# Kernel optimization log

Hardware: AMD Instinct MI355X
Metric: run time of the kernel (lower is better)

## Reference

```python
import jax, jax.numpy as jnp
import numpy as np

N_NODES = 100000
N_EDGES = 1600000
IN_F = 128
OUT_F = 64


def setup_inputs() -> dict:
    key = jax.random.key(0)
    k1, k2, k3, k4, k5, k6 = jax.random.split(key, 6)
    stdv = 1.0 / np.sqrt(OUT_F)
    return {
        "input": jax.random.normal(k1, (N_NODES, IN_F), dtype=jnp.float32),
        "weights": jax.random.uniform(k2, (IN_F, OUT_F), minval=-stdv, maxval=stdv, dtype=jnp.float32),
        "bias": jax.random.uniform(k3, (OUT_F,), minval=-stdv, maxval=stdv, dtype=jnp.float32),
        "adj_vals": jax.random.uniform(k4, (N_EDGES,), dtype=jnp.float32),
        "adj_rows": jax.random.randint(k5, (N_EDGES,), 0, N_NODES, dtype=jnp.int32),
        "adj_cols": jax.random.randint(k6, (N_EDGES,), 0, N_NODES, dtype=jnp.int32),
    }


def reference(input, weights, bias, adj_vals, adj_rows, adj_cols):
    # Dense transform: support = input @ W   -> [N, out_features]
    support = jnp.matmul(input, weights)
    # Sparse adjacency matmul (COO SpMM): out[r] += v * support[c]
    msgs = adj_vals[:, None] * support[adj_cols]          # [E, out_features]
    output = jax.ops.segment_sum(msgs, adj_rows, num_segments=N_NODES)
    # Fused bias epilogue
    return output + bias
```

## Files before the change

kernel.cpp:

```cpp
#include <hip/hip_runtime.h>
#include <hip/hip_bf16.h>

#define N_NODES 100000
#define IN_F 128
#define OUT_F 64
#define BROWS 64
#define NB 1563
#define BIN_TILE 4096
#define CSB_CAP 2048

__device__ __forceinline__ unsigned short f2bf(float x) {
    unsigned u = __float_as_uint(x);
    u += 0x7FFFu + ((u >> 16) & 1u);
    return (unsigned short)(u >> 16);
}
__device__ __forceinline__ float bf2f(unsigned short s) {
    return __uint_as_float(((unsigned)s) << 16);
}

__global__ __launch_bounds__(256) void gemm_count_kernel(
    const float* __restrict__ in, const float* __restrict__ W,
    unsigned short* __restrict__ support,
    const int* __restrict__ rows, int* __restrict__ cnt,
    int nE, int gemmBlocks)
{
    __shared__ float Alds[64 * 129];
    __shared__ int histL[NB];
    const int t = threadIdx.x;

    if ((int)blockIdx.x >= gemmBlocks) {
        for (int i = t; i < NB; i += 256) histL[i] = 0;
        __syncthreads();
        const int cb = blockIdx.x - gemmBlocks;
        for (int e = cb * 256 + t; e < nE; e += 256 * 256)
            atomicAdd(&histL[rows[e] >> 6], 1);
        __syncthreads();
        for (int i = t; i < NB; i += 256) {
            int h = histL[i];
            if (h) atomicAdd(&cnt[i], h);
        }
        return;
    }

    const long row0 = (long)blockIdx.x * 64;

    #pragma unroll
    for (int i = 0; i < 8; ++i) {
        int fi = t + i * 256;
        int r  = fi >> 5;
        int k4 = (fi & 31) << 2;
        float4 v = make_float4(0.f, 0.f, 0.f, 0.f);
        if (row0 + r < N_NODES)
            v = *(const float4*)(in + (row0 + r) * IN_F + k4);
        Alds[r * 129 + k4 + 0] = v.x;
        Alds[r * 129 + k4 + 1] = v.y;
        Alds[r * 129 + k4 + 2] = v.z;
        Alds[r * 129 + k4 + 3] = v.w;
    }
    __syncthreads();

    const int lane = t & 63;
    const int c0   = __builtin_amdgcn_readfirstlane((t >> 6) << 4);
    const float* __restrict__ Wp = W + c0;

    float acc[16];
    #pragma unroll
    for (int i = 0; i < 16; ++i) acc[i] = 0.f;

    const float* Ar = Alds + lane * 129;
    for (int k = 0; k < IN_F; ++k) {
        const float a = Ar[k];
        const float4 w0 = *(const float4*)(Wp + k * OUT_F + 0);
        const float4 w1 = *(const float4*)(Wp + k * OUT_F + 4);
        const float4 w2 = *(const float4*)(Wp + k * OUT_F + 8);
        const float4 w3 = *(const float4*)(Wp + k * OUT_F + 12);
        acc[0]  = fmaf(a, w0.x, acc[0]);  acc[1]  = fmaf(a, w0.y, acc[1]);
        acc[2]  = fmaf(a, w0.z, acc[2]);  acc[3]  = fmaf(a, w0.w, acc[3]);
        acc[4]  = fmaf(a, w1.x, acc[4]);  acc[5]  = fmaf(a, w1.y, acc[5]);
        acc[6]  = fmaf(a, w1.z, acc[6]);  acc[7]  = fmaf(a, w1.w, acc[7]);
        acc[8]  = fmaf(a, w2.x, acc[8]);  acc[9]  = fmaf(a, w2.y, acc[9]);
        acc[10] = fmaf(a, w2.z, acc[10]); acc[11] = fmaf(a, w2.w, acc[11]);
        acc[12] = fmaf(a, w3.x, acc[12]); acc[13] = fmaf(a, w3.y, acc[13]);
        acc[14] = fmaf(a, w3.z, acc[14]); acc[15] = fmaf(a, w3.w, acc[15]);
    }

    const long orow = row0 + lane;
    if (orow < N_NODES) {
        unsigned up[8];
        #pragma unroll
        for (int i = 0; i < 8; ++i)
            up[i] = (unsigned)f2bf(acc[2 * i]) |
                    ((unsigned)f2bf(acc[2 * i + 1]) << 16);
        unsigned short* o = support + orow * OUT_F + c0;
        *(uint4*)(o + 0) = make_uint4(up[0], up[1], up[2], up[3]);
        *(uint4*)(o + 8) = make_uint4(up[4], up[5], up[6], up[7]);
    }
}

__global__ __launch_bounds__(256) void zero_kernel(int* __restrict__ p, int n)
{
    int i = blockIdx.x * 256 + threadIdx.x;
    if (i < n) p[i] = 0;
}

__global__ __launch_bounds__(256) void scan_kernel(
    const int* __restrict__ cnt, int* __restrict__ base,
    int* __restrict__ cursor, int nE)
{
    __shared__ int lds[256];
    const int t = threadIdx.x;
    const int i0 = t * 8;
    int c[8];
    int tot = 0;
    #pragma unroll
    for (int k = 0; k < 8; ++k) {
        c[k] = (i0 + k < NB) ? cnt[i0 + k] : 0;
        tot += c[k];
    }

    lds[t] = tot;
    __syncthreads();
    int sum = tot;
    #pragma unroll
    for (int off = 1; off < 256; off <<= 1) {
        int y = (t >= off) ? lds[t - off] : 0;
        __syncthreads();
        sum += y;
        lds[t] = sum;
        __syncthreads();
    }
    int run = sum - tot;

    #pragma unroll
    for (int k = 0; k < 8; ++k) {
        if (i0 + k < NB) { base[i0 + k] = run; cursor[i0 + k] = run; }
        run += c[k];
    }
    if (t == 0) base[NB] = nE;
}

__global__ __launch_bounds__(256) void bin_kernel(
    const int* __restrict__ rows, const int* __restrict__ cols,
    const float* __restrict__ vals, int* __restrict__ cursor,
    uint2* __restrict__ binned, int nE)
{
    __shared__ int hist[NB];
    __shared__ int lbase[NB];
    const int t  = threadIdx.x;
    const int tb = blockIdx.x * BIN_TILE;

    for (int i = t; i < NB; i += 256) hist[i] = 0;
    __syncthreads();

    int myr[16], myrank[16];
    #pragma unroll
    for (int i = 0; i < 16; ++i) {
        int e = tb + i * 256 + t;
        if (e < nE) {
            int r = rows[e];
            myr[i] = r;
            myrank[i] = atomicAdd(&hist[r >> 6], 1);
        } else myr[i] = -1;
    }
    __syncthreads();

    for (int i = t; i < NB; i += 256) {
        int h = hist[i];
        lbase[i] = h ? atomicAdd(&cursor[i], h) : 0;
    }
    __syncthreads();

    #pragma unroll
    for (int i = 0; i < 16; ++i) {
        int e = tb + i * 256 + t;
        if (e < nE) {
            int r = myr[i];
            unsigned pack = ((unsigned)(r & (BROWS - 1)) << 17) | (unsigned)cols[e];
            binned[lbase[r >> 6] + myrank[i]] =
                make_uint2(pack, __float_as_uint(vals[e]));
        }
    }
}

__global__ __launch_bounds__(1024, 2) void csr_spmm(
    const int* __restrict__ base, const uint2* __restrict__ binned,
    const unsigned short* __restrict__ support, const float* __restrict__ bias,
    float* __restrict__ out)
{
    __shared__ uint2 stage[CSB_CAP];
    __shared__ uint2 sorted[CSB_CAP];
    __shared__ int rh[BROWS], rs[BROWS + 1], rc[BROWS];
    const int t = threadIdx.x;
    const int b = blockIdx.x;
    const int s = base[b], e = base[b + 1];
    const int n = e - s;
    const int wid  = t >> 6;
    const int lane = t & 63;
    const int row0 = b * BROWS;

    if (t < BROWS) rh[t] = 0;
    __syncthreads();

    if (n <= CSB_CAP) {
        for (int i = t; i < n; i += 1024) {
            uint2 p = binned[s + i];
            stage[i] = p;
            atomicAdd(&rh[p.x >> 17], 1);
        }
        __syncthreads();
        if (t < BROWS) {
            int v = rh[t];
            int inc = v;
            #pragma unroll
            for (int off = 1; off < BROWS; off <<= 1) {
                int y = __shfl_up(inc, off, 64);
                if (t >= off) inc += y;
            }
            rs[t] = inc - v;
            rc[t] = inc - v;
            if (t == BROWS - 1) rs[BROWS] = inc;
        }
        __syncthreads();
        for (int i = t; i < n; i += 1024) {
            uint2 p = stage[i];
            int pos = atomicAdd(&rc[p.x >> 17], 1);
            sorted[pos] = p;
        }
        __syncthreads();

        #pragma unroll
        for (int q = 0; q < 4; ++q) {
            const int rr = wid * 4 + q;
            const int r  = row0 + rr;
            if (r >= N_NODES) break;
            float acc = bias[lane];
            int j  = rs[rr];
            const int je = rs[rr + 1];
            for (; j + 7 < je; j += 8) {
                uint2 q0 = sorted[j + 0];
                uint2 q1 = sorted[j + 1];
                uint2 q2 = sorted[j + 2];
                uint2 q3 = sorted[j + 3];
                uint2 q4 = sorted[j + 4];
                uint2 q5 = sorted[j + 5];
                uint2 q6 = sorted[j + 6];
                uint2 q7 = sorted[j + 7];
                float g0 = bf2f(support[((size_t)(q0.x & 131071u) << 6) + lane]);
                float g1 = bf2f(support[((size_t)(q1.x & 131071u) << 6) + lane]);
                float g2 = bf2f(support[((size_t)(q2.x & 131071u) << 6) + lane]);
                float g3 = bf2f(support[((size_t)(q3.x & 131071u) << 6) + lane]);
                float g4 = bf2f(support[((size_t)(q4.x & 131071u) << 6) + lane]);
                float g5 = bf2f(support[((size_t)(q5.x & 131071u) << 6) + lane]);
                float g6 = bf2f(support[((size_t)(q6.x & 131071u) << 6) + lane]);
                float g7 = bf2f(support[((size_t)(q7.x & 131071u) << 6) + lane]);
                acc = fmaf(__uint_as_float(q0.y), g0, acc);
                acc = fmaf(__uint_as_float(q1.y), g1, acc);
                acc = fmaf(__uint_as_float(q2.y), g2, acc);
                acc = fmaf(__uint_as_float(q3.y), g3, acc);
                acc = fmaf(__uint_as_float(q4.y), g4, acc);
                acc = fmaf(__uint_as_float(q5.y), g5, acc);
                acc = fmaf(__uint_as_float(q6.y), g6, acc);
                acc = fmaf(__uint_as_float(q7.y), g7, acc);
            }
            for (; j < je; ++j) {
                uint2 p = sorted[j];
                acc = fmaf(__uint_as_float(p.y),
                           bf2f(support[((size_t)(p.x & 131071u) << 6) + lane]),
                           acc);
            }
            out[(size_t)r * OUT_F + lane] = acc;
        }
    } else {
        #pragma unroll
        for (int q = 0; q < 4; ++q) {
            const int rr = wid * 4 + q;
            const int r  = row0 + rr;
            if (r >= N_NODES) break;
            float acc = bias[lane];
            for (int j = s; j < e; ++j) {
                uint2 p = binned[j];
                if ((int)(p.x >> 17) == rr)
                    acc = fmaf(__uint_as_float(p.y),
                               bf2f(support[((size_t)(p.x & 131071u) << 6) + lane]),
                               acc);
            }
            out[(size_t)r * OUT_F + lane] = acc;
        }
    }
}

__global__ __launch_bounds__(256) void bias_init_kernel(
    float* __restrict__ out, const float* __restrict__ bias, int total4)
{
    const float4* b4 = (const float4*)bias;
    float4* o4 = (float4*)out;
    int i = blockIdx.x * blockDim.x + threadIdx.x;
    int stride = gridDim.x * blockDim.x;
    for (; i < total4; i += stride)
        o4[i] = b4[i & 15];
}

__global__ __launch_bounds__(256) void scatter_kernel(
    const float* __restrict__ vals, const int* __restrict__ rows,
    const int* __restrict__ cols, const unsigned short* __restrict__ support,
    float* __restrict__ out, int nE)
{
    const int e = blockIdx.x * 4 + (threadIdx.x >> 6);
    if (e >= nE) return;
    const int f = threadIdx.x & 63;
    const float m = vals[e] * bf2f(support[(size_t)cols[e] * OUT_F + f]);
    atomicAdd(&out[(size_t)rows[e] * OUT_F + f], m);
}

extern "C" void kernel_launch(void* const* d_in, const int* in_sizes, int n_in,
                              void* d_out, int out_size, void* d_ws, size_t ws_size,
                              hipStream_t stream) {
    const float* input    = (const float*)d_in[0];
    const float* weights  = (const float*)d_in[1];
    const float* bias     = (const float*)d_in[2];
    const float* adj_vals = (const float*)d_in[3];
    const int*   adj_rows = (const int*)d_in[4];
    const int*   adj_cols = (const int*)d_in[5];
    const int nE = in_sizes[3];

    float* out = (float*)d_out;
    const int gemmBlocks = (N_NODES + 63) / 64;

    char* ws = (char*)d_ws;
    const size_t off_support = 0;
    const size_t off_base    = 12800000;
    const size_t off_cursor  = off_base + 6400;
    const size_t off_binned  = off_cursor + 6400;
    const size_t required    = off_binned + (size_t)nE * 8;

    unsigned short* support = (unsigned short*)(ws + off_support);
    int*   bbase   = (int*)  (ws + off_base);
    int*   cursor  = (int*)  (ws + off_cursor);
    uint2* binned  = (uint2*)(ws + off_binned);

    if (ws_size >= required) {
        hipLaunchKernelGGL(zero_kernel, dim3((NB + 255) / 256), dim3(256),
                           0, stream, cursor, NB);
        hipLaunchKernelGGL(gemm_count_kernel, dim3(gemmBlocks + 256), dim3(256),
                           0, stream, input, weights, support,
                           adj_rows, cursor, nE, gemmBlocks);
        hipLaunchKernelGGL(scan_kernel, dim3(1), dim3(256), 0, stream,
                           cursor, bbase, cursor, nE);
        hipLaunchKernelGGL(bin_kernel, dim3((nE + BIN_TILE - 1) / BIN_TILE),
                           dim3(256), 0, stream,
                           adj_rows, adj_cols, adj_vals, cursor, binned, nE);
        hipLaunchKernelGGL(csr_spmm, dim3(NB), dim3(1024), 0, stream,
                           bbase, binned, support, bias, out);
    } else {
        hipLaunchKernelGGL(gemm_count_kernel, dim3(gemmBlocks), dim3(256),
                           0, stream, input, weights, support,
                           adj_rows, (int*)nullptr, nE, gemmBlocks);
        hipLaunchKernelGGL(bias_init_kernel, dim3(2048), dim3(256), 0, stream,
                           out, bias, N_NODES * OUT_F / 4);
        hipLaunchKernelGGL(scatter_kernel, dim3((nE + 3) / 4), dim3(256),
                           0, stream, adj_vals, adj_rows, adj_cols, support,
                           out, nE);
    }
}
```

Measured before the change: 134.3 us.

## Fuse GEMM with binning pass and split counting into its own kernel

Moves the edge histogram into a standalone count kernel that runs before the GEMM. The binning pass then runs in the same grid as the dense GEMM blocks, so the scatter-heavy binning overlaps with the compute-bound transform. The GEMM's LDS tile changes to a 132-float padded stride, which allows float4 stores and float4 reads of A. The zero kernel is replaced by hipMemsetAsync. In exchange, the count pass is now serialized ahead of the GEMM, and the shared LDS buffer is sized for the GEMM tile.

```diff
diff --git a/kernel.cpp b/kernel.cpp
--- a/kernel.cpp
+++ b/kernel.cpp
@@ -8,6 +8,7 @@
 #define NB 1563
 #define BIN_TILE 4096
 #define CSB_CAP 2048
+#define ASTRIDE 132
 
 __device__ __forceinline__ unsigned short f2bf(float x) {
     unsigned u = __float_as_uint(x);
@@ -18,44 +19,122 @@
     return __uint_as_float(((unsigned)s) << 16);
 }
 
-__global__ __launch_bounds__(256) void gemm_count_kernel(
+__global__ __launch_bounds__(256) void count_kernel(
+    const int* __restrict__ rows, int* __restrict__ cnt, int nE)
+{
+    __shared__ int hist[NB];
+    const int t = threadIdx.x;
+    for (int i = t; i < NB; i += 256) hist[i] = 0;
+    __syncthreads();
+
+    for (int e = blockIdx.x * 256 + t; e < nE; e += gridDim.x * 256)
+        atomicAdd(&hist[rows[e] >> 6], 1);
+    __syncthreads();
+
+    for (int i = t; i < NB; i += 256) {
+        int h = hist[i];
+        if (h) atomicAdd(&cnt[i], h);
+    }
+}
+
+__global__ __launch_bounds__(256) void scan_kernel(
+    const int* __restrict__ cnt, int* __restrict__ base,
+    int* __restrict__ cursor, int nE)
+{
+    __shared__ int lds[256];
+    const int t = threadIdx.x;
+    const int i0 = t * 8;
+    int c[8];
+    int tot = 0;
+    #pragma unroll
+    for (int k = 0; k < 8; ++k) {
+        c[k] = (i0 + k < NB) ? cnt[i0 + k] : 0;
+        tot += c[k];
+    }
+
+    lds[t] = tot;
+    __syncthreads();
+    int sum = tot;
+    #pragma unroll
+    for (int off = 1; off < 256; off <<= 1) {
+        int y = (t >= off) ? lds[t - off] : 0;
+        __syncthreads();
+        sum += y;
+        lds[t] = sum;
+        __syncthreads();
+    }
+    int run = sum - tot;
+
+    #pragma unroll
+    for (int k = 0; k < 8; ++k) {
+        if (i0 + k < NB) { base[i0 + k] = run; cursor[i0 + k] = run; }
+        run += c[k];
+    }
+    if (t == 0) base[NB] = nE;
+}
+
+__global__ __launch_bounds__(256) void gemm_bin_kernel(
     const float* __restrict__ in, const float* __restrict__ W,
     unsigned short* __restrict__ support,
-    const int* __restrict__ rows, int* __restrict__ cnt,
-    int nE, int gemmBlocks)
-{
-    __shared__ float Alds[64 * 129];
-    __shared__ int histL[NB];
+    const int* __restrict__ rows, const int* __restrict__ cols,
+    const float* __restrict__ vals, int* __restrict__ cursor,
+    uint2* __restrict__ binned, int nE, int gemmBlocks)
+{
+    __shared__ __align__(16) char smem[64 * ASTRIDE * 4];
     const int t = threadIdx.x;
 
     if ((int)blockIdx.x >= gemmBlocks) {
-        for (int i = t; i < NB; i += 256) histL[i] = 0;
-        __syncthreads();
-        const int cb = blockIdx.x - gemmBlocks;
-        for (int e = cb * 256 + t; e < nE; e += 256 * 256)
-            atomicAdd(&histL[rows[e] >> 6], 1);
-        __syncthreads();
+        int* hist  = (int*)smem;
+        int* lbase = hist + NB;
+        const int tb = (blockIdx.x - gemmBlocks) * BIN_TILE;
+
+        for (int i = t; i < NB; i += 256) hist[i] = 0;
+        __syncthreads();
+
+        int myr[16], myrank[16];
+        #pragma unroll
+        for (int i = 0; i < 16; ++i) {
+            int e = tb + i * 256 + t;
+            if (e < nE) {
+                int r = rows[e];
+                myr[i] = r;
+                myrank[i] = atomicAdd(&hist[r >> 6], 1);
+            } else myr[i] = -1;
+        }
+        __syncthreads();
+
         for (int i = t; i < NB; i += 256) {
-            int h = histL[i];
-            if (h) atomicAdd(&cnt[i], h);
+            int h = hist[i];
+            lbase[i] = h ? atomicAdd(&cursor[i], h) : 0;
+        }
+        __syncthreads();
+
+        #pragma unroll
+        for (int i = 0; i < 16; ++i) {
+            int e = tb + i * 256 + t;
+            if (e < nE) {
+                int r = myr[i];
+                unsigned pack = ((unsigned)(r & (BROWS - 1)) << 17)
+                              | (unsigned)cols[e];
+                binned[lbase[r >> 6] + myrank[i]] =
+                    make_uint2(pack, __float_as_uint(vals[e]));
+            }
         }
         return;
     }
 
+    float* Alds = (float*)smem;
     const long row0 = (long)blockIdx.x * 64;
 
     #pragma unroll
     for (int i = 0; i < 8; ++i) {
         int fi = t + i * 256;
         int r  = fi >> 5;
-        int k4 = (fi & 31) << 2;
+        int c4 = (fi & 31) << 2;
         float4 v = make_float4(0.f, 0.f, 0.f, 0.f);
         if (row0 + r < N_NODES)
-            v = *(const float4*)(in + (row0 + r) * IN_F + k4);
-        Alds[r * 129 + k4 + 0] = v.x;
-        Alds[r * 129 + k4 + 1] = v.y;
-        Alds[r * 129 + k4 + 2] = v.z;
-        Alds[r * 129 + k4 + 3] = v.w;
+            v = *(const float4*)(in + (row0 + r) * IN_F + c4);
+        *(float4*)(Alds + r * ASTRIDE + c4) = v;
     }
     __syncthreads();
 
@@ -67,21 +146,28 @@
     #pragma unroll
     for (int i = 0; i < 16; ++i) acc[i] = 0.f;
 
-    const float* Ar = Alds + lane * 129;
-    for (int k = 0; k < IN_F; ++k) {
-        const float a = Ar[k];
-        const float4 w0 = *(const float4*)(Wp + k * OUT_F + 0);
-        const float4 w1 = *(const float4*)(Wp + k * OUT_F + 4);
-        const float4 w2 = *(const float4*)(Wp + k * OUT_F + 8);
-        const float4 w3 = *(const float4*)(Wp + k * OUT_F + 12);
-        acc[0]  = fmaf(a, w0.x, acc[0]);  acc[1]  = fmaf(a, w0.y, acc[1]);
-        acc[2]  = fmaf(a, w0.z, acc[2]);  acc[3]  = fmaf(a, w0.w, acc[3]);
-        acc[4]  = fmaf(a, w1.x, acc[4]);  acc[5]  = fmaf(a, w1.y, acc[5]);
-        acc[6]  = fmaf(a, w1.z, acc[6]);  acc[7]  = fmaf(a, w1.w, acc[7]);
-        acc[8]  = fmaf(a, w2.x, acc[8]);  acc[9]  = fmaf(a, w2.y, acc[9]);
-        acc[10] = fmaf(a, w2.z, acc[10]); acc[11] = fmaf(a, w2.w, acc[11]);
-        acc[12] = fmaf(a, w3.x, acc[12]); acc[13] = fmaf(a, w3.y, acc[13]);
-        acc[14] = fmaf(a, w3.z, acc[14]); acc[15] = fmaf(a, w3.w, acc[15]);
+    const float* Ar = Alds + lane * ASTRIDE;
+    #pragma unroll 4
+    for (int k4 = 0; k4 < IN_F; k4 += 4) {
+        const float4 av = *(const float4*)(Ar + k4);
+        #pragma unroll
+        for (int j = 0; j < 4; ++j) {
+            const float a = (j == 0) ? av.x : (j == 1) ? av.y
+                           : (j == 2) ? av.z : av.w;
+            const int k = k4 + j;
+            const float4 w0 = *(const float4*)(Wp + k * OUT_F + 0);
+            const float4 w1 = *(const float4*)(Wp + k * OUT_F + 4);
+            const float4 w2 = *(const float4*)(Wp + k * OUT_F + 8);
+            const float4 w3 = *(const float4*)(Wp + k * OUT_F + 12);
+            acc[0]  = fmaf(a, w0.x, acc[0]);  acc[1]  = fmaf(a, w0.y, acc[1]);
+            acc[2]  = fmaf(a, w0.z, acc[2]);  acc[3]  = fmaf(a, w0.w, acc[3]);
+            acc[4]  = fmaf(a, w1.x, acc[4]);  acc[5]  = fmaf(a, w1.y, acc[5]);
+            acc[6]  = fmaf(a, w1.z, acc[6]);  acc[7]  = fmaf(a, w1.w, acc[7]);
+            acc[8]  = fmaf(a, w2.x, acc[8]);  acc[9]  = fmaf(a, w2.y, acc[9]);
+            acc[10] = fmaf(a, w2.z, acc[10]); acc[11] = fmaf(a, w2.w, acc[11]);
+            acc[12] = fmaf(a, w3.x, acc[12]); acc[13] = fmaf(a, w3.y, acc[13]);
+            acc[14] = fmaf(a, w3.z, acc[14]); acc[15] = fmaf(a, w3.w, acc[15]);
+        }
     }
 
     const long orow = row0 + lane;
@@ -94,91 +180,6 @@
         unsigned short* o = support + orow * OUT_F + c0;
         *(uint4*)(o + 0) = make_uint4(up[0], up[1], up[2], up[3]);
         *(uint4*)(o + 8) = make_uint4(up[4], up[5], up[6], up[7]);
-    }
-}
-
-__global__ __launch_bounds__(256) void zero_kernel(int* __restrict__ p, int n)
-{
-    int i = blockIdx.x * 256 + threadIdx.x;
-    if (i < n) p[i] = 0;
-}
-
-__global__ __launch_bounds__(256) void scan_kernel(
-    const int* __restrict__ cnt, int* __restrict__ base,
-    int* __restrict__ cursor, int nE)
-{
-    __shared__ int lds[256];
-    const int t = threadIdx.x;
-    const int i0 = t * 8;
-    int c[8];
-    int tot = 0;
-    #pragma unroll
-    for (int k = 0; k < 8; ++k) {
-        c[k] = (i0 + k < NB) ? cnt[i0 + k] : 0;
-        tot += c[k];
-    }
-
-    lds[t] = tot;
-    __syncthreads();
-    int sum = tot;
-    #pragma unroll
-    for (int off = 1; off < 256; off <<= 1) {
-        int y = (t >= off) ? lds[t - off] : 0;
-        __syncthreads();
-        sum += y;
-        lds[t] = sum;
-        __syncthreads();
-    }
-    int run = sum - tot;
-
-    #pragma unroll
-    for (int k = 0; k < 8; ++k) {
-        if (i0 + k < NB) { base[i0 + k] = run; cursor[i0 + k] = run; }
-        run += c[k];
-    }
-    if (t == 0) base[NB] = nE;
-}
-
-__global__ __launch_bounds__(256) void bin_kernel(
-    const int* __restrict__ rows, const int* __restrict__ cols,
-    const float* __restrict__ vals, int* __restrict__ cursor,
-    uint2* __restrict__ binned, int nE)
-{
-    __shared__ int hist[NB];
-    __shared__ int lbase[NB];
-    const int t  = threadIdx.x;
-    const int tb = blockIdx.x * BIN_TILE;
-
-    for (int i = t; i < NB; i += 256) hist[i] = 0;
-    __syncthreads();
-
-    int myr[16], myrank[16];
-    #pragma unroll
-    for (int i = 0; i < 16; ++i) {
-        int e = tb + i * 256 + t;
-        if (e < nE) {
-            int r = rows[e];
-            myr[i] = r;
-            myrank[i] = atomicAdd(&hist[r >> 6], 1);
-        } else myr[i] = -1;
-    }
-    __syncthreads();
-
-    for (int i = t; i < NB; i += 256) {
-        int h = hist[i];
-        lbase[i] = h ? atomicAdd(&cursor[i], h) : 0;
-    }
-    __syncthreads();
-
-    #pragma unroll
-    for (int i = 0; i < 16; ++i) {
-        int e = tb + i * 256 + t;
-        if (e < nE) {
-            int r = myr[i];
-            unsigned pack = ((unsigned)(r & (BROWS - 1)) << 17) | (unsigned)cols[e];
-            binned[lbase[r >> 6] + myrank[i]] =
-                make_uint2(pack, __float_as_uint(vals[e]));
-        }
     }
 }
 
@@ -325,6 +326,7 @@
 
     float* out = (float*)d_out;
     const int gemmBlocks = (N_NODES + 63) / 64;
+    const int binBlocks  = (nE + BIN_TILE - 1) / BIN_TILE;
 
     char* ws = (char*)d_ws;
     const size_t off_support = 0;
@@ -339,22 +341,23 @@
     uint2* binned  = (uint2*)(ws + off_binned);
 
     if (ws_size >= required) {
-        hipLaunchKernelGGL(zero_kernel, dim3((NB + 255) / 256), dim3(256),
-                           0, stream, cursor, NB);
-        hipLaunchKernelGGL(gemm_count_kernel, dim3(gemmBlocks + 256), dim3(256),
-                           0, stream, input, weights, support,
-                           adj_rows, cursor, nE, gemmBlocks);
+        hipMemsetAsync(cursor, 0, NB * sizeof(int), stream);
+        hipLaunchKernelGGL(count_kernel, dim3(256), dim3(256), 0, stream,
+                           adj_rows, cursor, nE);
         hipLaunchKernelGGL(scan_kernel, dim3(1), dim3(256), 0, stream,
                            cursor, bbase, cursor, nE);
-        hipLaunchKernelGGL(bin_kernel, dim3((nE + BIN_TILE - 1) / BIN_TILE),
+        hipLaunchKernelGGL(gemm_bin_kernel, dim3(gemmBlocks + binBlocks),
                            dim3(256), 0, stream,
-                           adj_rows, adj_cols, adj_vals, cursor, binned, nE);
+                           input, weights, support,
+                           adj_rows, adj_cols, adj_vals, cursor, binned,
+                           nE, gemmBlocks);
         hipLaunchKernelGGL(csr_spmm, dim3(NB), dim3(1024), 0, stream,
                            bbase, binned, support, bias, out);
     } else {
-        hipLaunchKernelGGL(gemm_count_kernel, dim3(gemmBlocks), dim3(256),
+        hipLaunchKernelGGL(gemm_bin_kernel, dim3(gemmBlocks), dim3(256),
                            0, stream, input, weights, support,
-                           adj_rows, (int*)nullptr, nE, gemmBlocks);
+                           adj_rows, adj_cols, adj_vals, (int*)nullptr,
+                           (uint2*)nullptr, nE, gemmBlocks);
         hipLaunchKernelGGL(bias_init_kernel, dim3(2048), dim3(256), 0, stream,
                            out, bias, N_NODES * OUT_F / 4);
         hipLaunchKernelGGL(scatter_kernel, dim3((nE + 3) / 4), dim3(256),
```

Result: faster. 130.5 us (-2.8%).
